# Kernel tuning notes

Measured on AMD Instinct MI355X. Metric: run time of the kernel, lower is better.

The kernel has to match this reference:

```python
import jax, jax.numpy as jnp
import numpy as np

N = 100000   # nodes
E = 1600000  # edges (avg degree 16)
D = 64       # in_dim == hidden_dim
L = 3        # num_layers
EPS = 1e-5   # LayerNorm eps


def setup_inputs() -> dict:
    key = jax.random.key(0)
    k0, k1, k2 = jax.random.split(key, 3)
    x = jax.random.normal(k0, (N, D), dtype=jnp.float32)
    edge_index = jax.random.randint(k1, (2, E), 0, N, dtype=jnp.int32)
    # Per-layer GCN weights/bias (Glorot-ish scale) and LayerNorm params
    Ws = jax.random.normal(k2, (L, D, D), dtype=jnp.float32) / np.float32(np.sqrt(D))
    bs = jnp.zeros((L, D), dtype=jnp.float32)
    gammas = jnp.ones((L, D), dtype=jnp.float32)
    betas = jnp.zeros((L, D), dtype=jnp.float32)
    return {"x": x, "Ws": Ws, "bs": bs, "gammas": gammas, "betas": betas,
            "edge_index": edge_index}


def _layer_norm(h, gamma, beta):
    mu = jnp.mean(h, axis=-1, keepdims=True)
    var = jnp.mean(jnp.square(h - mu), axis=-1, keepdims=True)
    return (h - mu) * jax.lax.rsqrt(var + EPS) * gamma + beta


def reference(x, Ws, bs, gammas, betas, edge_index):
    # GCNConv semantics: add self-loops, symmetric deg^{-1/2} normalization.
    loop = jnp.arange(N, dtype=edge_index.dtype)
    row = jnp.concatenate([edge_index[0], loop])  # source (gather)
    col = jnp.concatenate([edge_index[1], loop])  # target (scatter)
    deg = jax.ops.segment_sum(jnp.ones_like(col, dtype=x.dtype), col, num_segments=N)
    dinv = jnp.where(deg > 0, jax.lax.rsqrt(deg), jnp.zeros_like(deg))
    enorm = dinv[row] * dinv[col]  # (E+N,)

    h = x
    for i in range(L):
        hw = h @ Ws[i]                                   # (N, D) small GEMM
        msg = hw[row] * enorm[:, None]                   # (E+N, D) gather
        h = jax.ops.segment_sum(msg, col, num_segments=N) + bs[i]  # scatter-add
        h = _layer_norm(h, gammas[i], betas[i])
        if i < L - 1:
            h = jax.nn.relu(h)                           # dropout is identity in eval
    return h
```

## Files before the change

### kernel.cpp

```cpp
#include <hip/hip_runtime.h>
#include <hip/hip_bf16.h>


#define DDIM 64
#define EPSV 1e-5f
#define BSHIFT 9
#define BNODES (1 << BSHIFT)
#define NBUCK 256
#define CHUNK 4096
#define CBLKS 256

typedef __hip_bfloat16 bf16;
typedef unsigned int u32;
typedef unsigned short u16;
typedef unsigned long long u64;
typedef __attribute__((ext_vector_type(8))) short frag8;
typedef __attribute__((ext_vector_type(4))) float f32x4;

__device__ __forceinline__ float b2f(bf16 v) { return __bfloat162float(v); }
__device__ __forceinline__ float lo2f(u32 u) {
    union { u32 x; float f; } c; c.x = u << 16; return c.f;
}
__device__ __forceinline__ float hi2f(u32 u) {
    union { u32 x; float f; } c; c.x = u & 0xffff0000u; return c.f;
}
__device__ __forceinline__ u32 packbf(float a, float b) {
    union { bf16 h; u16 u; } ca, cb;
    ca.h = __float2bfloat16(a);
    cb.h = __float2bfloat16(b);
    return (u32)ca.u | ((u32)cb.u << 16);
}
__device__ __forceinline__ float cvt_load(const void* src, int i, int f32) {
    return f32 ? ((const float*)src)[i] : b2f(((const bf16*)src)[i]);
}


__global__ void __launch_bounds__(256) bucket_count(const int* __restrict__ col,
                                                    int* __restrict__ partials,
                                                    const u32* __restrict__ g,
                                                    int* __restrict__ flagF32, int E) {
    __shared__ int h[NBUCK];
    int tid = threadIdx.x;
    if (blockIdx.x == 0 && tid == 0) *flagF32 = (g[0] == 0x3F800000u) ? 1 : 0;
    h[tid] = 0;
    __syncthreads();
    for (int i = blockIdx.x * blockDim.x + tid; i < E; i += gridDim.x * blockDim.x)
        atomicAdd(&h[col[i] >> BSHIFT], 1);
    __syncthreads();
    partials[blockIdx.x * NBUCK + tid] = h[tid];
}

__global__ void bucket_scan(const int* __restrict__ partials, int* __restrict__ bbase,
                            int* __restrict__ gcur, int nbuck, int E) {
    __shared__ int s[NBUCK];
    int tid = threadIdx.x;
    int v = 0;
    for (int b = 0; b < CBLKS; b++) v += partials[b * NBUCK + tid];
    s[tid] = v;
    __syncthreads();
    for (int off = 1; off < NBUCK; off <<= 1) {
        int t = (tid >= off) ? s[tid - off] : 0;
        __syncthreads();
        s[tid] += t;
        __syncthreads();
    }
    int excl = s[tid] - v;
    if (tid < nbuck) { bbase[tid] = excl; gcur[tid] = excl; }
    if (tid == 0) bbase[nbuck] = E;
}

__global__ void __launch_bounds__(256) partition_edges(const int* __restrict__ row,
                                                       const int* __restrict__ col,
                                                       int* __restrict__ gcur,
                                                       u64* __restrict__ pairs, int E) {
    __shared__ int hist[NBUCK];
    __shared__ int lbase[NBUCK];
    __shared__ int gdelta[NBUCK];
    __shared__ int lcur[NBUCK];
    __shared__ int sbuf[NBUCK];
    __shared__ int dest[CHUNK];
    __shared__ u64 stage[CHUNK];
    int tid = threadIdx.x;
    int chunk0 = blockIdx.x * CHUNK;
    hist[tid] = 0;
    lcur[tid] = 0;
    __syncthreads();
    int r[16], c[16];
#pragma unroll
    for (int i = 0; i < 16; i++) {
        int idx = chunk0 + i * 256 + tid;
        if (idx < E) {
            r[i] = row[idx];
            c[i] = col[idx];
            atomicAdd(&hist[c[i] >> BSHIFT], 1);
        }
    }
    __syncthreads();
    int h = hist[tid];
    sbuf[tid] = h;
    __syncthreads();
    for (int off = 1; off < 256; off <<= 1) {
        int t = (tid >= off) ? sbuf[tid - off] : 0;
        __syncthreads();
        sbuf[tid] += t;
        __syncthreads();
    }
    int excl = sbuf[tid] - h;
    lbase[tid] = excl;
    int gb = (h > 0) ? atomicAdd(&gcur[tid], h) : 0;
    gdelta[tid] = gb - excl;
    __syncthreads();
#pragma unroll
    for (int i = 0; i < 16; i++) {
        int idx = chunk0 + i * 256 + tid;
        if (idx < E) {
            int b = c[i] >> BSHIFT;
            int pos = lbase[b] + atomicAdd(&lcur[b], 1);
            stage[pos] = ((u64)(u32)c[i] << 32) | (u32)r[i];
            dest[pos] = gdelta[b];
        }
    }
    __syncthreads();
    int chunkN = min(CHUNK, E - chunk0);
    for (int j = tid; j < chunkN; j += 256)
        pairs[(size_t)(dest[j] + j)] = stage[j];
}

__global__ void __launch_bounds__(512) build_csr(const u64* __restrict__ pairs,
                                                 const int* __restrict__ bbase,
                                                 int* __restrict__ ptr,
                                                 int* __restrict__ srcs,
                                                 float* __restrict__ dinv,
                                                 int N, int E) {
    __shared__ int deg[BNODES];
    __shared__ int lptr[BNODES];
    __shared__ int lfill[BNODES];
    int b = blockIdx.x;
    int node0 = b << BSHIFT;
    int nn = min(BNODES, N - node0);
    int tid = threadIdx.x;
    deg[tid] = 0;
    lfill[tid] = 0;
    __syncthreads();
    int beg = bbase[b], end = bbase[b + 1];
    for (int i = beg + tid; i < end; i += 512)
        atomicAdd(&deg[(int)(pairs[i] >> 32) - node0], 1);
    __syncthreads();
    int d = deg[tid];
    lptr[tid] = d;
    __syncthreads();
    for (int off = 1; off < BNODES; off <<= 1) {
        int t = (tid >= off) ? lptr[tid - off] : 0;
        __syncthreads();
        lptr[tid] += t;
        __syncthreads();
    }
    int excl = lptr[tid] - d;
    lptr[tid] = beg + excl;
    if (tid < nn) {
        ptr[node0 + tid] = beg + excl;
        dinv[node0 + tid] = rsqrtf((float)(d + 1));
    }
    if (b == 0 && tid == 0) ptr[N] = E;
    __syncthreads();
    for (int i = beg + tid; i < end; i += 512) {
        u64 pr = pairs[i];
        int li = (int)(pr >> 32) - node0;
        int p = lptr[li] + atomicAdd(&lfill[li], 1);
        srcs[p] = (int)(pr & 0xffffffffu);
    }
}

__global__ void convert_all(const void* __restrict__ x, const void* __restrict__ W,
                            const void* __restrict__ b, const void* __restrict__ g,
                            const void* __restrict__ bt,
                            bf16* __restrict__ H, bf16* __restrict__ dWt,
                            bf16* __restrict__ db, bf16* __restrict__ dg,
                            bf16* __restrict__ dbt,
                            const int* __restrict__ flagF32,
                            const float* __restrict__ dinv, int nX, int nW, int nS) {
    int i = blockIdx.x * blockDim.x + threadIdx.x;
    int f = *flagF32;
    if (i < nX) { H[i] = __float2bfloat16(cvt_load(x, i, f) * dinv[i >> 6]); return; }
    i -= nX;
    if (i < nW) {
        int L = i >> 12, n = (i >> 6) & 63, k = i & 63;
        dWt[i] = __float2bfloat16(cvt_load(W, (L << 12) | (k << 6) | n, f));
        return;
    }
    i -= nW;
    if (i < nS) { db[i] = __float2bfloat16(cvt_load(b, i, f)); return; }
    i -= nS;
    if (i < nS) { dg[i] = __float2bfloat16(cvt_load(g, i, f)); return; }
    i -= nS;
    if (i < nS) { dbt[i] = __float2bfloat16(cvt_load(bt, i, f)); }
}


__global__ void __launch_bounds__(256, 5) fused_layer(const bf16* __restrict__ Hs,
                                                      const int* __restrict__ ptr,
                                                      const int* __restrict__ srcs,
                                                      const float* __restrict__ dinv,
                                                      const bf16* __restrict__ Wt,
                                                      const bf16* __restrict__ bias,
                                                      const bf16* __restrict__ gamma,
                                                      const bf16* __restrict__ beta,
                                                      bf16* __restrict__ outB,
                                                      float* __restrict__ outF,
                                                      const int* __restrict__ flagF32,
                                                      const float* __restrict__ dscale,
                                                      int relu, int last, int N) {
    __shared__ __align__(16) bf16 lsA[4][16][64];
    int tid = threadIdx.x;
    int wv = tid >> 6, lane = tid & 63;
    int half = lane >> 5, lane32 = lane & 31;
    int sub = lane32 >> 3, quad = lane & 7;
    int r0 = blockIdx.x * 64 + wv * 16;

    for (int it = 0; it < 8; it++) {
        int v = r0 + it * 2 + half;
        int vc = v < N ? v : N - 1;
        uint4 selfq = ((const uint4*)(Hs + ((size_t)vc << 6)))[quad];
        int beg = 0, end = 0;
        if (v < N) { beg = ptr[v]; end = ptr[v + 1]; }
        float a0 = 0.f, a1 = 0.f, a2 = 0.f, a3 = 0.f;
        float a4 = 0.f, a5 = 0.f, a6 = 0.f, a7 = 0.f;
        for (int base = beg; base < end; base += 32) {
            int rem = end - base;
            int m = rem < 32 ? rem : 32;
            int sidx = (lane32 < m) ? srcs[base + lane32] : 0;
            for (int j = 0; j < m; j += 8) {
                int e0 = j + sub;
                int e1 = j + 4 + sub;
                int s0 = __shfl(sidx, (half << 5) + e0, 64);
                int s1 = __shfl(sidx, (half << 5) + e1, 64);
                float k0 = (e0 < m) ? 1.f : 0.f;
                float k1 = (e1 < m) ? 1.f : 0.f;
                uint4 q0 = ((const uint4*)(Hs + ((size_t)s0 << 6)))[quad];
                uint4 q1 = ((const uint4*)(Hs + ((size_t)s1 << 6)))[quad];
                a0 = fmaf(lo2f(q0.x), k0, a0); a1 = fmaf(hi2f(q0.x), k0, a1);
                a2 = fmaf(lo2f(q0.y), k0, a2); a3 = fmaf(hi2f(q0.y), k0, a3);
                a4 = fmaf(lo2f(q0.z), k0, a4); a5 = fmaf(hi2f(q0.z), k0, a5);
                a6 = fmaf(lo2f(q0.w), k0, a6); a7 = fmaf(hi2f(q0.w), k0, a7);
                a0 = fmaf(lo2f(q1.x), k1, a0); a1 = fmaf(hi2f(q1.x), k1, a1);
                a2 = fmaf(lo2f(q1.y), k1, a2); a3 = fmaf(hi2f(q1.y), k1, a3);
                a4 = fmaf(lo2f(q1.z), k1, a4); a5 = fmaf(hi2f(q1.z), k1, a5);
                a6 = fmaf(lo2f(q1.w), k1, a6); a7 = fmaf(hi2f(q1.w), k1, a7);
            }
        }
#pragma unroll
        for (int d = 8; d < 32; d <<= 1) {
            a0 += __shfl_xor(a0, d, 64); a1 += __shfl_xor(a1, d, 64);
            a2 += __shfl_xor(a2, d, 64); a3 += __shfl_xor(a3, d, 64);
            a4 += __shfl_xor(a4, d, 64); a5 += __shfl_xor(a5, d, 64);
            a6 += __shfl_xor(a6, d, 64); a7 += __shfl_xor(a7, d, 64);
        }
        if (sub == 0 && v < N) {
            a0 += lo2f(selfq.x); a1 += hi2f(selfq.x);
            a2 += lo2f(selfq.y); a3 += hi2f(selfq.y);
            a4 += lo2f(selfq.z); a5 += hi2f(selfq.z);
            a6 += lo2f(selfq.w); a7 += hi2f(selfq.w);
            float dv = dinv[v];
            uint4 o;
            o.x = packbf(a0 * dv, a1 * dv);
            o.y = packbf(a2 * dv, a3 * dv);
            o.z = packbf(a4 * dv, a5 * dv);
            o.w = packbf(a6 * dv, a7 * dv);
            *(uint4*)&lsA[wv][it * 2 + half][quad * 8] = o;
        }
    }

    int n = lane & 15, q = lane >> 4;
    frag8 af0 = *(const frag8*)&lsA[wv][n][q * 8];
    frag8 af1 = *(const frag8*)&lsA[wv][n][32 + q * 8];

    f32x4 acc[4];
#pragma unroll
    for (int t = 0; t < 4; t++) acc[t] = (f32x4){0.f, 0.f, 0.f, 0.f};
#pragma unroll
    for (int t = 0; t < 4; t++) {
        const uint4* bp = (const uint4*)(Wt + (((size_t)(t * 16 + n)) << 6));
        frag8 bf0 = __builtin_bit_cast(frag8, bp[q]);
        frag8 bf1 = __builtin_bit_cast(frag8, bp[4 + q]);
        acc[t] = __builtin_amdgcn_mfma_f32_16x16x32_bf16(af0, bf0, acc[t], 0, 0, 0);
        acc[t] = __builtin_amdgcn_mfma_f32_16x16x32_bf16(af1, bf1, acc[t], 0, 0, 0);
    }

    float bb[4], gg[4], be[4];
#pragma unroll
    for (int t = 0; t < 4; t++) {
        int c = t * 16 + n;
        bb[t] = b2f(bias[c]);
        gg[t] = b2f(gamma[c]);
        be[t] = b2f(beta[c]);
    }
    int f32o = last ? flagF32[0] : 0;

#pragma unroll
    for (int r = 0; r < 4; r++) {
        int rr = r0 + q * 4 + r;
        float v0 = acc[0][r] + bb[0];
        float v1 = acc[1][r] + bb[1];
        float v2 = acc[2][r] + bb[2];
        float v3 = acc[3][r] + bb[3];
        float s = v0 + v1 + v2 + v3;
        s += __shfl_xor(s, 1, 64);
        s += __shfl_xor(s, 2, 64);
        s += __shfl_xor(s, 4, 64);
        s += __shfl_xor(s, 8, 64);
        float mu = s * (1.f / 64.f);
        float d0 = v0 - mu, d1 = v1 - mu, d2 = v2 - mu, d3 = v3 - mu;
        float sq = d0 * d0 + d1 * d1 + d2 * d2 + d3 * d3;
        sq += __shfl_xor(sq, 1, 64);
        sq += __shfl_xor(sq, 2, 64);
        sq += __shfl_xor(sq, 4, 64);
        sq += __shfl_xor(sq, 8, 64);
        float rs = rsqrtf(sq * (1.f / 64.f) + EPSV);
        float o0 = d0 * rs * gg[0] + be[0];
        float o1 = d1 * rs * gg[1] + be[1];
        float o2 = d2 * rs * gg[2] + be[2];
        float o3 = d3 * rs * gg[3] + be[3];
        if (relu) {
            o0 = fmaxf(o0, 0.f); o1 = fmaxf(o1, 0.f);
            o2 = fmaxf(o2, 0.f); o3 = fmaxf(o3, 0.f);
        }
        if (rr < N) {
            if (dscale) {
                float sc = dscale[rr];
                o0 *= sc; o1 *= sc; o2 *= sc; o3 *= sc;
            }
            size_t base = ((size_t)rr << 6) + n;
            if (f32o) {
                outF[base] = o0; outF[base + 16] = o1;
                outF[base + 32] = o2; outF[base + 48] = o3;
            } else {
                outB[base] = __float2bfloat16(o0);
                outB[base + 16] = __float2bfloat16(o1);
                outB[base + 32] = __float2bfloat16(o2);
                outB[base + 48] = __float2bfloat16(o3);
            }
        }
    }
}


extern "C" void kernel_launch(void* const* d_in, const int* in_sizes, int n_in,
                              void* d_out, int out_size, void* d_ws, size_t ws_size,
                              hipStream_t stream) {
    (void)n_in; (void)out_size; (void)ws_size;
    const void* x      = d_in[0];
    const void* Wsrc   = d_in[1];
    const void* bsrc   = d_in[2];
    const void* gsrc   = d_in[3];
    const void* btsrc  = d_in[4];
    const int*  ei     = (const int*)d_in[5];
    int N = in_sizes[0] / DDIM;
    int E = in_sizes[5] / 2;
    const int* rowp = ei;
    const int* colp = ei + E;

    char* w = (char*)d_ws;
    auto alloc = [&](size_t bytes) -> char* {
        char* p = w;
        w += (bytes + 255) / 256 * 256;
        return p;
    };
    int*   flag  = (int*)alloc(4);
    int*   gcur  = (int*)alloc(NBUCK * 4);
    int*   parts = (int*)alloc((size_t)CBLKS * NBUCK * 4);
    int*   bbase = (int*)alloc((NBUCK + 1) * 4);
    int*   ptr   = (int*)alloc((size_t)(N + 1) * 4);
    int*   srcs  = (int*)alloc((size_t)E * 4);
    float* dinv  = (float*)alloc((size_t)N * 4);
    char*  hreg  = alloc((size_t)N * DDIM * 2);
    bf16*  H     = (bf16*)hreg;
    u64*   pairs = (u64*)hreg;
    bf16*  wsW   = (bf16*)alloc((size_t)3 * 4096 * 2);
    bf16*  wsB   = (bf16*)alloc(192 * 2);
    bf16*  wsG   = (bf16*)alloc(192 * 2);
    bf16*  wsBt  = (bf16*)alloc(192 * 2);
    bf16*  H2    = (bf16*)alloc((size_t)N * DDIM * 2);

    const int tb = 256;
    int nbuck = (N + BNODES - 1) >> BSHIFT;
    bucket_count<<<CBLKS, tb, 0, stream>>>(colp, parts, (const u32*)gsrc, flag, E);
    bucket_scan<<<1, NBUCK, 0, stream>>>(parts, bbase, gcur, nbuck, E);
    partition_edges<<<(E + CHUNK - 1) / CHUNK, tb, 0, stream>>>(rowp, colp, gcur, pairs, E);
    build_csr<<<nbuck, 512, 0, stream>>>(pairs, bbase, ptr, srcs, dinv, N, E);

    int nX = N * DDIM, nW = 3 * 4096, nS = 192;
    int nAll = nX + nW + 3 * nS;
    convert_all<<<(nAll + tb - 1) / tb, tb, 0, stream>>>(x, Wsrc, bsrc, gsrc, btsrc,
                                                         H, wsW, wsB, wsG, wsBt,
                                                         flag, dinv, nX, nW, nS);

    int gBlocks = (N + 63) / 64;
    fused_layer<<<gBlocks, tb, 0, stream>>>(H, ptr, srcs, dinv,
                                            wsW + 0 * 4096, wsB + 0,   wsG + 0,   wsBt + 0,
                                            H2, nullptr, flag, dinv, 1, 0, N);
    fused_layer<<<gBlocks, tb, 0, stream>>>(H2, ptr, srcs, dinv,
                                            wsW + 1 * 4096, wsB + 64,  wsG + 64,  wsBt + 64,
                                            H, nullptr, flag, dinv, 1, 0, N);
    fused_layer<<<gBlocks, tb, 0, stream>>>(H, ptr, srcs, dinv,
                                            wsW + 2 * 4096, wsB + 128, wsG + 128, wsBt + 128,
                                            (bf16*)d_out, (float*)d_out, flag, nullptr, 0, 1, N);
}
```

Measured before the change: 257.4 us.

## Fuse input conversion into CSR build and prefetch first neighbor chunk per row

Removes the separate convert_all launch. The bf16 scaling of x by deg^-1/2 now happens inside build_csr using the shared-memory degree counts, and one extra block converts the weights and LayerNorm parameters. In fused_layer, each wave loads ptr/dinv for its 16 rows once and prefetches the first 32 source indices of all 8 rows before the gather loop, then runs an unrolled first-chunk path, so more independent loads are in flight. The pairs buffer no longer aliases H, which costs extra workspace. build_csr blocks also do the x conversion, lengthening that phase.

```diff
diff --git a/kernel.cpp b/kernel.cpp
--- a/kernel.cpp
+++ b/kernel.cpp
@@ -131,14 +131,38 @@
                                                  int* __restrict__ ptr,
                                                  int* __restrict__ srcs,
                                                  float* __restrict__ dinv,
-                                                 int N, int E) {
+                                                 const void* __restrict__ x,
+                                                 const void* __restrict__ W,
+                                                 const void* __restrict__ bsv,
+                                                 const void* __restrict__ gsv,
+                                                 const void* __restrict__ btv,
+                                                 bf16* __restrict__ H,
+                                                 bf16* __restrict__ dWt,
+                                                 bf16* __restrict__ db,
+                                                 bf16* __restrict__ dg,
+                                                 bf16* __restrict__ dbt,
+                                                 const int* __restrict__ flagF32,
+                                                 int nbuck, int N, int E) {
     __shared__ int deg[BNODES];
     __shared__ int lptr[BNODES];
     __shared__ int lfill[BNODES];
     int b = blockIdx.x;
+    int tid = threadIdx.x;
+    if (b >= nbuck) {
+        int f = *flagF32;
+        for (int i = tid; i < 3 * 4096; i += 512) {
+            int L = i >> 12, n = (i >> 6) & 63, k = i & 63;
+            dWt[i] = __float2bfloat16(cvt_load(W, (L << 12) | (k << 6) | n, f));
+        }
+        for (int i = tid; i < 192; i += 512) {
+            db[i]  = __float2bfloat16(cvt_load(bsv, i, f));
+            dg[i]  = __float2bfloat16(cvt_load(gsv, i, f));
+            dbt[i] = __float2bfloat16(cvt_load(btv, i, f));
+        }
+        return;
+    }
     int node0 = b << BSHIFT;
     int nn = min(BNODES, N - node0);
-    int tid = threadIdx.x;
     deg[tid] = 0;
     lfill[tid] = 0;
     __syncthreads();
@@ -169,31 +193,12 @@
         int p = lptr[li] + atomicAdd(&lfill[li], 1);
         srcs[p] = (int)(pr & 0xffffffffu);
     }
-}
-
-__global__ void convert_all(const void* __restrict__ x, const void* __restrict__ W,
-                            const void* __restrict__ b, const void* __restrict__ g,
-                            const void* __restrict__ bt,
-                            bf16* __restrict__ H, bf16* __restrict__ dWt,
-                            bf16* __restrict__ db, bf16* __restrict__ dg,
-                            bf16* __restrict__ dbt,
-                            const int* __restrict__ flagF32,
-                            const float* __restrict__ dinv, int nX, int nW, int nS) {
-    int i = blockIdx.x * blockDim.x + threadIdx.x;
     int f = *flagF32;
-    if (i < nX) { H[i] = __float2bfloat16(cvt_load(x, i, f) * dinv[i >> 6]); return; }
-    i -= nX;
-    if (i < nW) {
-        int L = i >> 12, n = (i >> 6) & 63, k = i & 63;
-        dWt[i] = __float2bfloat16(cvt_load(W, (L << 12) | (k << 6) | n, f));
-        return;
-    }
-    i -= nW;
-    if (i < nS) { db[i] = __float2bfloat16(cvt_load(b, i, f)); return; }
-    i -= nS;
-    if (i < nS) { dg[i] = __float2bfloat16(cvt_load(g, i, f)); return; }
-    i -= nS;
-    if (i < nS) { dbt[i] = __float2bfloat16(cvt_load(bt, i, f)); }
+    for (int i = tid; i < (nn << 6); i += 512) {
+        float dv = rsqrtf((float)(deg[i >> 6] + 1));
+        int gi = (node0 << 6) + i;
+        H[gi] = __float2bfloat16(cvt_load(x, gi, f) * dv);
+    }
 }
 
 
@@ -217,25 +222,70 @@
     int sub = lane32 >> 3, quad = lane & 7;
     int r0 = blockIdx.x * 64 + wv * 16;
 
+    int myrow = r0 + (lane & 15);
+    int mb = 0, me = 0;
+    float mdv = 0.f;
+    if (myrow < N) {
+        mb = ptr[myrow];
+        me = ptr[myrow + 1];
+        mdv = dinv[myrow];
+    }
+
+    int sid0[8];
+#pragma unroll
     for (int it = 0; it < 8; it++) {
-        int v = r0 + it * 2 + half;
+        int rl = it * 2 + half;
+        int pb = __shfl(mb, rl, 64);
+        int dd = __shfl(me, rl, 64) - pb;
+        int s = 0;
+        if (lane32 < dd) s = srcs[pb + lane32];
+        sid0[it] = s;
+    }
+
+#pragma unroll
+    for (int it = 0; it < 8; it++) {
+        int rl = it * 2 + half;
+        int v = r0 + rl;
         int vc = v < N ? v : N - 1;
         uint4 selfq = ((const uint4*)(Hs + ((size_t)vc << 6)))[quad];
-        int beg = 0, end = 0;
-        if (v < N) { beg = ptr[v]; end = ptr[v + 1]; }
+        int beg = __shfl(mb, rl, 64);
+        int end = __shfl(me, rl, 64);
+        int m = end - beg;
+        if (m > 32) m = 32;
+        int sidx = sid0[it];
         float a0 = 0.f, a1 = 0.f, a2 = 0.f, a3 = 0.f;
         float a4 = 0.f, a5 = 0.f, a6 = 0.f, a7 = 0.f;
-        for (int base = beg; base < end; base += 32) {
+#pragma unroll
+        for (int j = 0; j < 32; j += 8) {
+            int e0 = j + sub;
+            int e1 = j + 4 + sub;
+            int s0 = __shfl(sidx, (half << 5) + e0, 64);
+            int s1 = __shfl(sidx, (half << 5) + e1, 64);
+            float k0 = (e0 < m) ? 1.f : 0.f;
+            float k1 = (e1 < m) ? 1.f : 0.f;
+            uint4 q0 = ((const uint4*)(Hs + ((size_t)s0 << 6)))[quad];
+            uint4 q1 = ((const uint4*)(Hs + ((size_t)s1 << 6)))[quad];
+            a0 = fmaf(lo2f(q0.x), k0, a0); a1 = fmaf(hi2f(q0.x), k0, a1);
+            a2 = fmaf(lo2f(q0.y), k0, a2); a3 = fmaf(hi2f(q0.y), k0, a3);
+            a4 = fmaf(lo2f(q0.z), k0, a4); a5 = fmaf(hi2f(q0.z), k0, a5);
+            a6 = fmaf(lo2f(q0.w), k0, a6); a7 = fmaf(hi2f(q0.w), k0, a7);
+            a0 = fmaf(lo2f(q1.x), k1, a0); a1 = fmaf(hi2f(q1.x), k1, a1);
+            a2 = fmaf(lo2f(q1.y), k1, a2); a3 = fmaf(hi2f(q1.y), k1, a3);
+            a4 = fmaf(lo2f(q1.z), k1, a4); a5 = fmaf(hi2f(q1.z), k1, a5);
+            a6 = fmaf(lo2f(q1.w), k1, a6); a7 = fmaf(hi2f(q1.w), k1, a7);
+        }
+        for (int base = beg + 32; base < end; base += 32) {
             int rem = end - base;
-            int m = rem < 32 ? rem : 32;
-            int sidx = (lane32 < m) ? srcs[base + lane32] : 0;
-            for (int j = 0; j < m; j += 8) {
+            int m2 = rem < 32 ? rem : 32;
+            int sx = 0;
+            if (lane32 < m2) sx = srcs[base + lane32];
+            for (int j = 0; j < m2; j += 8) {
                 int e0 = j + sub;
                 int e1 = j + 4 + sub;
-                int s0 = __shfl(sidx, (half << 5) + e0, 64);
-                int s1 = __shfl(sidx, (half << 5) + e1, 64);
-                float k0 = (e0 < m) ? 1.f : 0.f;
-                float k1 = (e1 < m) ? 1.f : 0.f;
+                int s0 = __shfl(sx, (half << 5) + e0, 64);
+                int s1 = __shfl(sx, (half << 5) + e1, 64);
+                float k0 = (e0 < m2) ? 1.f : 0.f;
+                float k1 = (e1 < m2) ? 1.f : 0.f;
                 uint4 q0 = ((const uint4*)(Hs + ((size_t)s0 << 6)))[quad];
                 uint4 q1 = ((const uint4*)(Hs + ((size_t)s1 << 6)))[quad];
                 a0 = fmaf(lo2f(q0.x), k0, a0); a1 = fmaf(hi2f(q0.x), k0, a1);
@@ -255,18 +305,18 @@
             a4 += __shfl_xor(a4, d, 64); a5 += __shfl_xor(a5, d, 64);
             a6 += __shfl_xor(a6, d, 64); a7 += __shfl_xor(a7, d, 64);
         }
+        float dv = __shfl(mdv, rl, 64);
         if (sub == 0 && v < N) {
             a0 += lo2f(selfq.x); a1 += hi2f(selfq.x);
             a2 += lo2f(selfq.y); a3 += hi2f(selfq.y);
             a4 += lo2f(selfq.z); a5 += hi2f(selfq.z);
             a6 += lo2f(selfq.w); a7 += hi2f(selfq.w);
-            float dv = dinv[v];
             uint4 o;
             o.x = packbf(a0 * dv, a1 * dv);
             o.y = packbf(a2 * dv, a3 * dv);
             o.z = packbf(a4 * dv, a5 * dv);
             o.w = packbf(a6 * dv, a7 * dv);
-            *(uint4*)&lsA[wv][it * 2 + half][quad * 8] = o;
+            *(uint4*)&lsA[wv][rl][quad * 8] = o;
         }
     }
 
@@ -372,9 +422,8 @@
     int*   ptr   = (int*)alloc((size_t)(N + 1) * 4);
     int*   srcs  = (int*)alloc((size_t)E * 4);
     float* dinv  = (float*)alloc((size_t)N * 4);
-    char*  hreg  = alloc((size_t)N * DDIM * 2);
-    bf16*  H     = (bf16*)hreg;
-    u64*   pairs = (u64*)hreg;
+    bf16*  H     = (bf16*)alloc((size_t)N * DDIM * 2);
+    u64*   pairs = (u64*)alloc((size_t)E * 8);
     bf16*  wsW   = (bf16*)alloc((size_t)3 * 4096 * 2);
     bf16*  wsB   = (bf16*)alloc(192 * 2);
     bf16*  wsG   = (bf16*)alloc(192 * 2);
@@ -386,13 +435,10 @@
     bucket_count<<<CBLKS, tb, 0, stream>>>(colp, parts, (const u32*)gsrc, flag, E);
     bucket_scan<<<1, NBUCK, 0, stream>>>(parts, bbase, gcur, nbuck, E);
     partition_edges<<<(E + CHUNK - 1) / CHUNK, tb, 0, stream>>>(rowp, colp, gcur, pairs, E);
-    build_csr<<<nbuck, 512, 0, stream>>>(pairs, bbase, ptr, srcs, dinv, N, E);
-
-    int nX = N * DDIM, nW = 3 * 4096, nS = 192;
-    int nAll = nX + nW + 3 * nS;
-    convert_all<<<(nAll + tb - 1) / tb, tb, 0, stream>>>(x, Wsrc, bsrc, gsrc, btsrc,
-                                                         H, wsW, wsB, wsG, wsBt,
-                                                         flag, dinv, nX, nW, nS);
+    build_csr<<<nbuck + 1, 512, 0, stream>>>(pairs, bbase, ptr, srcs, dinv,
+                                             x, Wsrc, bsrc, gsrc, btsrc,
+                                             H, wsW, wsB, wsG, wsBt,
+                                             flag, nbuck, N, E);
 
     int gBlocks = (N + 63) / 64;
     fused_layer<<<gBlocks, tb, 0, stream>>>(H, ptr, srcs, dinv,
```

After: 291.6 us. 1.13x slower.
